# Optimization experiments

Measured on AMD Instinct MI355X. Metric: run time of the kernel, lower is better.

## Reference

```python
import jax, jax.numpy as jnp
import numpy as np

N = 50000   # nodes
E = 640000  # edges (before self-loops)
D = 128     # in_dim == out_dim
H = 4       # heads
C = 32      # per-head channels (out_dim // heads)
ED = 1      # edge_dim
NEG_SLOPE = 0.2
LN_EPS = 1e-5


def setup_inputs() -> dict:
    key = jax.random.key(0)
    ks = jax.random.split(key, 8)
    glorot = lambda k, sh, fan: jax.random.normal(k, sh, jnp.float32) / np.float32(np.sqrt(fan))
    return dict(
        x=jax.random.normal(ks[0], (N, D), jnp.float32),
        edge_index=jax.random.randint(ks[1], (2, E), 0, N, dtype=jnp.int32),
        edge_attr=jax.random.uniform(ks[2], (E, ED), jnp.float32),
        W_l=glorot(ks[3], (D, H * C), D), b_l=jnp.zeros((H * C,), jnp.float32),
        W_r=glorot(ks[4], (D, H * C), D), b_r=jnp.zeros((H * C,), jnp.float32),
        W_e=glorot(ks[5], (ED, H * C), ED),
        att=glorot(ks[6], (H, C), C),
        bias=jnp.zeros((H * C,), jnp.float32),
        ln_gamma=jnp.ones((H * C,), jnp.float32),
        ln_beta=jnp.zeros((H * C,), jnp.float32),
    )


def reference(x, edge_index, edge_attr, W_l, b_l, W_r, b_r, W_e, att, bias, ln_gamma, ln_beta):
    n = x.shape[0]
    src, dst = edge_index[0], edge_index[1]
    # --- add self loops; self-loop edge_attr = mean of incoming attrs (PyG fill_value='mean') ---
    attr_sum = jax.ops.segment_sum(edge_attr, dst, num_segments=n)          # (N, ED)
    cnt = jax.ops.segment_sum(jnp.ones((edge_attr.shape[0], 1), edge_attr.dtype), dst, num_segments=n)
    loop_attr = attr_sum / jnp.maximum(cnt, 1.0)
    ea = jnp.concatenate([edge_attr, loop_attr], axis=0)                    # (E+N, ED)
    loop = jnp.arange(n, dtype=src.dtype)
    src = jnp.concatenate([src, loop])
    dst = jnp.concatenate([dst, loop])
    # --- GATv2: separate source/target linear transforms ---
    x_l = (x @ W_l + b_l).reshape(n, H, C)   # source (x_j)
    x_r = (x @ W_r + b_r).reshape(n, H, C)   # target (x_i)
    e_f = (ea @ W_e).reshape(-1, H, C)       # edge embedding (E+N, H, C)
    xj = x_l[src]                            # gather (E+N, H, C)
    m = jax.nn.leaky_relu(xj + x_r[dst] + e_f, NEG_SLOPE)
    alpha = jnp.einsum('ehc,hc->eh', m, att)
    # --- segment softmax over incoming edges of each target node ---
    amax = jax.ops.segment_max(alpha, dst, num_segments=n)  # every node has a self-loop
    ex = jnp.exp(alpha - amax[dst])
    denom = jax.ops.segment_sum(ex, dst, num_segments=n)
    a = ex / denom[dst]                                     # (E+N, H); attn dropout is eval no-op
    # --- scatter-aggregate messages, concat heads, conv bias ---
    out = jax.ops.segment_sum(xj * a[..., None], dst, num_segments=n).reshape(n, H * C) + bias
    # --- ELU, dropout (eval no-op), residual (in_dim == out_dim, no res_proj), LayerNorm ---
    out = jax.nn.elu(out) + x
    mu = jnp.mean(out, axis=-1, keepdims=True)
    var = jnp.var(out, axis=-1, keepdims=True)
    return (out - mu) * jax.lax.rsqrt(var + LN_EPS) * ln_gamma + ln_beta
```

## Files before the change

kernel.cpp:

```cpp
#include <hip/hip_runtime.h>
#include <hip/hip_fp16.h>
#include <math.h>

#define DCH 128
#define NEG 0.2f
#define LOG2E 1.44269504088896f
#define NPART 256
#define SCAP 20
#define BCAP 1152

typedef _Float16 f16x8 __attribute__((ext_vector_type(8)));
typedef float    f32x4 __attribute__((ext_vector_type(4)));
typedef float    f32x2 __attribute__((ext_vector_type(2)));
typedef unsigned long long u64;

static __device__ __forceinline__ float dpp_radd4(float v) {
    int b;
    b = __builtin_amdgcn_update_dpp(0, __float_as_int(v), 0xB1, 0xF, 0xF, true);
    v += __int_as_float(b);
    b = __builtin_amdgcn_update_dpp(0, __float_as_int(v), 0x4E, 0xF, 0xF, true);
    v += __int_as_float(b);
    return v;
}

__global__ __launch_bounds__(256) void k_prep(
        const float* __restrict__ x, __half* __restrict__ xf16, int total4,
        const float* __restrict__ Wl, const float* __restrict__ Wr,
        __half* __restrict__ wtl, __half* __restrict__ wtr, int nb_cvt) {
    int bid = blockIdx.x;
    if (bid < nb_cvt) {
        int i = bid * 256 + (int)threadIdx.x;
        if (i >= total4) return;
        float4 v = ((const float4*)x)[i];
        __half2* dst = (__half2*)xf16 + 2 * (size_t)i;
        dst[0] = __floats2half2_rn(v.x, v.y);
        dst[1] = __floats2half2_rn(v.z, v.w);
    } else {
        int t = (bid - nb_cvt) * 256 + (int)threadIdx.x;
        if (t >= 2 * DCH * DCH) return;
        const float* W = (t < DCH * DCH) ? Wl : Wr;
        __half* wt = (t < DCH * DCH) ? wtl : wtr;
        int u = t & (DCH * DCH - 1);
        int k = u >> 7, j = u & 127;
        wt[j * 128 + k] = __float2half_rn(W[u]);
    }
}

__global__ __launch_bounds__(256) void k_mmpart(
        const __half* __restrict__ xf16,
        const __half* __restrict__ wtl, const __half* __restrict__ wtr,
        const float* __restrict__ bl, const float* __restrict__ br,
        __half* __restrict__ xl16, float* __restrict__ xro, int N,
        const int* __restrict__ ei, const float* __restrict__ eattr,
        unsigned* __restrict__ sorted, unsigned* __restrict__ cnt,
        int E, int NB, int chunkE, int nb_mm) {
    if ((int)blockIdx.x >= nb_mm) {
        __shared__ unsigned cur[1024];
        int p = (int)blockIdx.x - nb_mm;
        for (int i = threadIdx.x; i < 1024; i += 256) cur[i] = 0u;
        __syncthreads();
        int e0 = p * chunkE;
        int e1 = e0 + chunkE; if (e1 > E) e1 = E;
        for (int e = e0 + (int)threadIdx.x; e < e1; e += 256) {
            int d = ei[E + e], s = ei[e];
            float a = eattr[e];
            int b = d >> 6, dl = d & 63;
            unsigned q = (unsigned)fminf(a * 1024.f + 0.5f, 1023.f);
            unsigned rank = atomicAdd(&cur[b], 1u);
            if (rank < SCAP)
                sorted[((size_t)b * NPART + p) * SCAP + rank] =
                    (unsigned)dl | ((unsigned)s << 6) | (q << 22);
        }
        __syncthreads();
        for (int b = threadIdx.x; b < NB; b += 256) {
            unsigned c = cur[b];
            cnt[(size_t)b * NPART + p] = c < SCAP ? c : SCAP;
        }
        return;
    }
    int wave = threadIdx.x >> 6, lane = threadIdx.x & 63;
    int node0 = blockIdx.x * 64;
    int jbase = wave * 32;
    int rl = lane & 15, kg = lane >> 4;
    f32x4 acc[4][2][2];
    #pragma unroll
    for (int a = 0; a < 4; ++a)
        #pragma unroll
        for (int b = 0; b < 2; ++b)
            #pragma unroll
            for (int c = 0; c < 2; ++c)
                acc[a][b][c] = (f32x4){0.f, 0.f, 0.f, 0.f};
    #pragma unroll
    for (int ks = 0; ks < 4; ++ks) {
        int koff = ks * 32 + kg * 8;
        f16x8 av[4];
        #pragma unroll
        for (int rt = 0; rt < 4; ++rt) {
            int row = node0 + rt * 16 + rl;
            if (row >= N) row = N - 1;
            av[rt] = *(const f16x8*)(xf16 + (size_t)row * 128 + koff);
        }
        #pragma unroll
        for (int jt = 0; jt < 2; ++jt) {
            int j = jbase + jt * 16 + rl;
            size_t ob = (size_t)j * 128 + koff;
            f16x8 bL = *(const f16x8*)(wtl + ob);
            f16x8 bR = *(const f16x8*)(wtr + ob);
            #pragma unroll
            for (int rt = 0; rt < 4; ++rt) {
                acc[rt][jt][0] = __builtin_amdgcn_mfma_f32_16x16x32_f16(av[rt], bL, acc[rt][jt][0], 0, 0, 0);
                acc[rt][jt][1] = __builtin_amdgcn_mfma_f32_16x16x32_f16(av[rt], bR, acc[rt][jt][1], 0, 0, 0);
            }
        }
    }
    float blv[2], brv[2];
    #pragma unroll
    for (int jt = 0; jt < 2; ++jt) {
        int j = jbase + jt * 16 + rl;
        blv[jt] = bl[j]; brv[jt] = br[j];
    }
    #pragma unroll
    for (int rt = 0; rt < 4; ++rt) {
        #pragma unroll
        for (int r = 0; r < 4; ++r) {
            int row = node0 + rt * 16 + kg * 4 + r;
            if (row < N) {
                #pragma unroll
                for (int jt = 0; jt < 2; ++jt) {
                    int j = jbase + jt * 16 + rl;
                    xl16[(size_t)row * 128 + j] = __float2half_rn(acc[rt][jt][0][r] + blv[jt]);
                    xro[(size_t)row * 128 + j] = acc[rt][jt][1][r] + brv[jt];
                }
            }
        }
    }
}

__global__ __launch_bounds__(256) void k_fill2(
        const unsigned* __restrict__ sorted, const unsigned* __restrict__ cnt,
        unsigned* __restrict__ csr, uint2* __restrict__ ndesc,
        float* __restrict__ lattr, int N) {
    __shared__ unsigned lraw[BCAP];
    __shared__ unsigned hcnt[64], qsum[64];
    __shared__ unsigned wsum[4], wpre[5];
    __shared__ int ncur[64];
    __shared__ int tot_s;
    int t = threadIdx.x, lane = t & 63, w = t >> 6;
    int bucket = blockIdx.x;
    if (t < 64) { hcnt[t] = 0u; qsum[t] = 0u; }
    unsigned v = cnt[(size_t)bucket * NPART + t];
    int sc = (int)v;
    #pragma unroll
    for (int o = 1; o < 64; o <<= 1) {
        int tmp = __shfl_up(sc, o, 64);
        if (lane >= o) sc += tmp;
    }
    if (lane == 63) wsum[w] = (unsigned)sc;
    __syncthreads();
    if (t == 0) {
        wpre[0] = 0;
        #pragma unroll
        for (int k = 0; k < 4; ++k) wpre[k + 1] = wpre[k] + wsum[k];
        tot_s = (int)(wpre[4] < BCAP ? wpre[4] : BCAP);
    }
    __syncthreads();
    unsigned sb = wpre[w] + (unsigned)sc - v;
    {
        const unsigned* src = sorted + ((size_t)bucket * NPART + t) * SCAP;
        for (int i = 0; i < (int)v; ++i) {
            unsigned idx = sb + (unsigned)i;
            if (idx < BCAP) {
                unsigned rec = src[i];
                lraw[idx] = rec;
                int dl = (int)(rec & 63u);
                atomicAdd(&hcnt[dl], 1u);
                atomicAdd(&qsum[dl], rec >> 22);
            }
        }
    }
    __syncthreads();
    if (t < 64) {
        int nv = (int)hcnt[t], nsc = nv;
        #pragma unroll
        for (int o = 1; o < 64; o <<= 1) {
            int tmp = __shfl_up(nsc, o, 64);
            if (t >= o) nsc += tmp;
        }
        int nb = nsc - nv;
        ncur[t] = nb;
        int node = bucket * 64 + t;
        if (node < N) {
            ndesc[node] = make_uint2((unsigned)(bucket * BCAP + nb), (unsigned)nv);
            lattr[node] = ((float)qsum[t] * (1.f / 1024.f)) / fmaxf((float)nv, 1.f);
        }
    }
    __syncthreads();
    int tot = tot_s;
    for (int i = t; i < tot; i += 256) {
        unsigned rec = lraw[i];
        int dl = (int)(rec & 63u);
        int pos = atomicAdd(&ncur[dl], 1);
        csr[(size_t)bucket * BCAP + pos] = ((rec >> 6) & 0xFFFFu) | ((rec >> 22) << 16);
    }
}

__global__ __launch_bounds__(256) void k_gat(
        const __half* __restrict__ xl16, const float* __restrict__ xrp, const float* __restrict__ x,
        const unsigned* __restrict__ csr, const uint2* __restrict__ ndesc,
        const float* __restrict__ lattr,
        const float* __restrict__ We, const float* __restrict__ att, const float* __restrict__ bias,
        const float* __restrict__ gamma, const float* __restrict__ beta,
        float* __restrict__ out, int N) {
    int wid = threadIdx.x >> 6;
    int lane = threadIdx.x & 63;
    int node = blockIdx.x * 4 + wid;
    if (node >= N) return;
    int q = lane >> 4;
    int sl = lane & 15;
    int c8 = sl << 3;

    float4 attA = *(const float4*)(att + c8);
    float4 attB = *(const float4*)(att + c8 + 4);
    attA.x *= LOG2E; attA.y *= LOG2E; attA.z *= LOG2E; attA.w *= LOG2E;
    attB.x *= LOG2E; attB.y *= LOG2E; attB.z *= LOG2E; attB.w *= LOG2E;
    float4 weA = *(const float4*)(We + c8);
    float4 weB = *(const float4*)(We + c8 + 4);
    float4 xrA = *(const float4*)(xrp + (size_t)node * 128 + c8);
    float4 xrB = *(const float4*)(xrp + (size_t)node * 128 + c8 + 4);

    uint2 nd = ndesc[node];
    int beg = (int)nd.x, deg = (int)nd.y;
    float la = lattr[node];
    int T = deg + 1;

    float4 accA = {0.f, 0.f, 0.f, 0.f}, accB = {0.f, 0.f, 0.f, 0.f};
    float den = 0.f;

    for (int p = 0; p < T; p += 4) {
        int idx = p + q;
        bool isReal = idx < deg;
        unsigned rec = 0u;
        if (isReal) rec = csr[beg + idx];
        int src = isReal ? (int)(rec & 0xFFFFu) : node;
        float ea = isReal ? (float)(rec >> 16) * (1.f / 1024.f) : la;
        float vmask = (idx <= deg) ? 1.f : 0.f;
        uint4 graw = *(const uint4*)(xl16 + ((size_t)src << 7) + c8);
        float2 g0 = __half22float2(*(const __half2*)&graw.x);
        float2 g1 = __half22float2(*(const __half2*)&graw.y);
        float2 g2 = __half22float2(*(const __half2*)&graw.z);
        float2 g3 = __half22float2(*(const __half2*)&graw.w);
        float t0 = g0.x + fmaf(ea, weA.x, xrA.x); t0 = fmaxf(t0, t0 * NEG);
        float t1 = g0.y + fmaf(ea, weA.y, xrA.y); t1 = fmaxf(t1, t1 * NEG);
        float t2 = g1.x + fmaf(ea, weA.z, xrA.z); t2 = fmaxf(t2, t2 * NEG);
        float t3 = g1.y + fmaf(ea, weA.w, xrA.w); t3 = fmaxf(t3, t3 * NEG);
        float t4 = g2.x + fmaf(ea, weB.x, xrB.x); t4 = fmaxf(t4, t4 * NEG);
        float t5 = g2.y + fmaf(ea, weB.y, xrB.y); t5 = fmaxf(t5, t5 * NEG);
        float t6 = g3.x + fmaf(ea, weB.z, xrB.z); t6 = fmaxf(t6, t6 * NEG);
        float t7 = g3.y + fmaf(ea, weB.w, xrB.w); t7 = fmaxf(t7, t7 * NEG);
        float d = t0 * attA.x;
        d = fmaf(t1, attA.y, d); d = fmaf(t2, attA.z, d); d = fmaf(t3, attA.w, d);
        d = fmaf(t4, attB.x, d); d = fmaf(t5, attB.y, d); d = fmaf(t6, attB.z, d);
        d = fmaf(t7, attB.w, d);
        float pt = dpp_radd4(d);
        float pe = exp2f(pt) * vmask;
        den += pe;
        accA.x = fmaf(pe, g0.x, accA.x); accA.y = fmaf(pe, g0.y, accA.y);
        accA.z = fmaf(pe, g1.x, accA.z); accA.w = fmaf(pe, g1.y, accA.w);
        accB.x = fmaf(pe, g2.x, accB.x); accB.y = fmaf(pe, g2.y, accB.y);
        accB.z = fmaf(pe, g3.x, accB.z); accB.w = fmaf(pe, g3.y, accB.w);
    }

    den += __shfl_xor(den, 16, 64);
    accA.x += __shfl_xor(accA.x, 16, 64); accA.y += __shfl_xor(accA.y, 16, 64);
    accA.z += __shfl_xor(accA.z, 16, 64); accA.w += __shfl_xor(accA.w, 16, 64);
    accB.x += __shfl_xor(accB.x, 16, 64); accB.y += __shfl_xor(accB.y, 16, 64);
    accB.z += __shfl_xor(accB.z, 16, 64); accB.w += __shfl_xor(accB.w, 16, 64);
    den += __shfl_xor(den, 32, 64);
    accA.x += __shfl_xor(accA.x, 32, 64); accA.y += __shfl_xor(accA.y, 32, 64);
    accA.z += __shfl_xor(accA.z, 32, 64); accA.w += __shfl_xor(accA.w, 32, 64);
    accB.x += __shfl_xor(accB.x, 32, 64); accB.y += __shfl_xor(accB.y, 32, 64);
    accB.z += __shfl_xor(accB.z, 32, 64); accB.w += __shfl_xor(accB.w, 32, 64);

    float inv = 1.f / den;
    float4 biA = *(const float4*)(bias + c8);
    float4 biB = *(const float4*)(bias + c8 + 4);
    float o0 = fmaf(accA.x, inv, biA.x), o1 = fmaf(accA.y, inv, biA.y);
    float o2 = fmaf(accA.z, inv, biA.z), o3 = fmaf(accA.w, inv, biA.w);
    float o4 = fmaf(accB.x, inv, biB.x), o5 = fmaf(accB.y, inv, biB.y);
    float o6 = fmaf(accB.z, inv, biB.z), o7 = fmaf(accB.w, inv, biB.w);
    o0 = o0 > 0.f ? o0 : (__expf(o0) - 1.f);
    o1 = o1 > 0.f ? o1 : (__expf(o1) - 1.f);
    o2 = o2 > 0.f ? o2 : (__expf(o2) - 1.f);
    o3 = o3 > 0.f ? o3 : (__expf(o3) - 1.f);
    o4 = o4 > 0.f ? o4 : (__expf(o4) - 1.f);
    o5 = o5 > 0.f ? o5 : (__expf(o5) - 1.f);
    o6 = o6 > 0.f ? o6 : (__expf(o6) - 1.f);
    o7 = o7 > 0.f ? o7 : (__expf(o7) - 1.f);
    float4 xvA = *(const float4*)(x + (size_t)node * 128 + c8);
    float4 xvB = *(const float4*)(x + (size_t)node * 128 + c8 + 4);
    o0 += xvA.x; o1 += xvA.y; o2 += xvA.z; o3 += xvA.w;
    o4 += xvB.x; o5 += xvB.y; o6 += xvB.z; o7 += xvB.w;
    float r1 = ((o0 + o1) + (o2 + o3)) + ((o4 + o5) + (o6 + o7));
    float r2 = o0 * o0;
    r2 = fmaf(o1, o1, r2); r2 = fmaf(o2, o2, r2); r2 = fmaf(o3, o3, r2);
    r2 = fmaf(o4, o4, r2); r2 = fmaf(o5, o5, r2); r2 = fmaf(o6, o6, r2);
    r2 = fmaf(o7, o7, r2);
    #pragma unroll
    for (int mk = 1; mk < 16; mk <<= 1) {
        r1 += __shfl_xor(r1, mk, 16);
        r2 += __shfl_xor(r2, mk, 16);
    }
    float mean = r1 * (1.f / 128.f);
    float var  = r2 * (1.f / 128.f) - mean * mean;
    float rr = rsqrtf(var + 1e-5f);
    if (q == 0) {
        float4 gmA = *(const float4*)(gamma + c8);
        float4 gmB = *(const float4*)(gamma + c8 + 4);
        float4 btA = *(const float4*)(beta + c8);
        float4 btB = *(const float4*)(beta + c8 + 4);
        float4 wA, wB;
        wA.x = (o0 - mean) * rr * gmA.x + btA.x;
        wA.y = (o1 - mean) * rr * gmA.y + btA.y;
        wA.z = (o2 - mean) * rr * gmA.z + btA.z;
        wA.w = (o3 - mean) * rr * gmA.w + btA.w;
        wB.x = (o4 - mean) * rr * gmB.x + btB.x;
        wB.y = (o5 - mean) * rr * gmB.y + btB.y;
        wB.z = (o6 - mean) * rr * gmB.z + btB.z;
        wB.w = (o7 - mean) * rr * gmB.w + btB.w;
        *(float4*)(out + (size_t)node * 128 + c8) = wA;
        *(float4*)(out + (size_t)node * 128 + c8 + 4) = wB;
    }
}

extern "C" void kernel_launch(void* const* d_in, const int* in_sizes, int n_in,
                              void* d_out, int out_size, void* d_ws, size_t ws_size,
                              hipStream_t stream) {
    const float* x     = (const float*)d_in[0];
    const int*   ei    = (const int*)d_in[1];
    const float* eattr = (const float*)d_in[2];
    const float* Wl    = (const float*)d_in[3];
    const float* bl    = (const float*)d_in[4];
    const float* Wr    = (const float*)d_in[5];
    const float* br    = (const float*)d_in[6];
    const float* We    = (const float*)d_in[7];
    const float* att   = (const float*)d_in[8];
    const float* bias  = (const float*)d_in[9];
    const float* gam   = (const float*)d_in[10];
    const float* bet   = (const float*)d_in[11];
    float* out = (float*)d_out;
    int N = in_sizes[0] / DCH;
    int E = in_sizes[1] / 2;
    int NB = (N + 63) / 64;

    char* base = (char*)d_ws;
    size_t off = 0;
    auto alloc = [&](size_t nbytes) -> void* {
        void* p = base + off;
        off += (nbytes + 255) & ~(size_t)255;
        return p;
    };
    unsigned* sorted = (unsigned*)alloc((size_t)NB * NPART * SCAP * 4);
    unsigned* cnt    = (unsigned*)alloc((size_t)NB * NPART * 4);
    unsigned* csr    = (unsigned*)alloc((size_t)NB * BCAP * 4);
    uint2*    ndesc  = (uint2*)alloc((size_t)N * 8);
    float*    lattr  = (float*)alloc((size_t)N * 4);
    __half*   xl16   = (__half*)alloc((size_t)N * DCH * 2);
    float*    xrb    = (float*)alloc((size_t)N * DCH * 4);
    __half*   xf16   = (__half*)alloc((size_t)N * DCH * 2);
    __half*   wtl    = (__half*)alloc((size_t)DCH * DCH * 2);
    __half*   wtr    = (__half*)alloc((size_t)DCH * DCH * 2);
    (void)n_in; (void)out_size; (void)ws_size;

    int total4  = N * DCH / 4;
    int nb_cvt  = (total4 + 255) / 256;
    int nb_cvtw = (2 * DCH * DCH + 255) / 256;
    int nb_mm   = (N + 63) / 64;
    int chunkE  = (E + NPART - 1) / NPART;

    k_prep<<<nb_cvt + nb_cvtw, 256, 0, stream>>>(
        x, xf16, total4, Wl, Wr, wtl, wtr, nb_cvt);
    k_mmpart<<<nb_mm + NPART, 256, 0, stream>>>(
        xf16, wtl, wtr, bl, br, xl16, xrb, N,
        ei, eattr, sorted, cnt, E, NB, chunkE, nb_mm);
    k_fill2<<<NB, 256, 0, stream>>>(
        sorted, cnt, csr, ndesc, lattr, N);
    k_gat<<<(N + 3) / 4, 256, 0, stream>>>(
        xl16, xrb, x, csr, ndesc, lattr, We, att, bias, gam, bet, out, N);
}
```

Measured before the change: 98.76 us.

## Compact partition records via local counting sort and prefetch gathers in GAT loop

The partition blocks now run a two-pass local counting sort in shared memory: they count records per bucket, prefix-sum the counts, write records contiguously into an LDS buffer, and copy that buffer to global memory in one coalesced pass. A per-(bucket,partition) base-offset array replaces the fixed SCAP-slot layout, so the padded, scattered writes go away and per-slot overflow truncation is no longer possible. The GAT edge loop is also software-pipelined, with edge metadata prefetched four iterations ahead and feature gathers three ahead, to hide gather latency. This costs about 22KB more LDS per partition block and extra registers in k_gat, which may lower occupancy.

```diff
diff --git a/kernel.cpp b/kernel.cpp
--- a/kernel.cpp
+++ b/kernel.cpp
@@ -6,13 +6,11 @@
 #define NEG 0.2f
 #define LOG2E 1.44269504088896f
 #define NPART 256
-#define SCAP 20
+#define RCAP 2512
 #define BCAP 1152
 
 typedef _Float16 f16x8 __attribute__((ext_vector_type(8)));
 typedef float    f32x4 __attribute__((ext_vector_type(4)));
-typedef float    f32x2 __attribute__((ext_vector_type(2)));
-typedef unsigned long long u64;
 
 static __device__ __forceinline__ float dpp_radd4(float v) {
     int b;
@@ -53,29 +51,68 @@
         __half* __restrict__ xl16, float* __restrict__ xro, int N,
         const int* __restrict__ ei, const float* __restrict__ eattr,
         unsigned* __restrict__ sorted, unsigned* __restrict__ cnt,
+        unsigned* __restrict__ gbase,
         int E, int NB, int chunkE, int nb_mm) {
     if ((int)blockIdx.x >= nb_mm) {
-        __shared__ unsigned cur[1024];
+        __shared__ unsigned lcnt[1024];
+        __shared__ unsigned lbase[1024];
+        __shared__ unsigned lcur[1024];
+        __shared__ unsigned recbuf[RCAP];
+        __shared__ unsigned wsum2[4], wpre2[5];
         int p = (int)blockIdx.x - nb_mm;
-        for (int i = threadIdx.x; i < 1024; i += 256) cur[i] = 0u;
+        int t = threadIdx.x, lane = t & 63, w = t >> 6;
+        for (int i = t; i < 1024; i += 256) lcnt[i] = 0u;
         __syncthreads();
         int e0 = p * chunkE;
         int e1 = e0 + chunkE; if (e1 > E) e1 = E;
-        for (int e = e0 + (int)threadIdx.x; e < e1; e += 256) {
+        for (int e = e0 + t; e < e1; e += 256)
+            atomicAdd(&lcnt[ei[E + e] >> 6], 1u);
+        __syncthreads();
+        unsigned c0 = lcnt[t * 4 + 0], c1 = lcnt[t * 4 + 1];
+        unsigned c2 = lcnt[t * 4 + 2], c3 = lcnt[t * 4 + 3];
+        unsigned s4 = c0 + c1 + c2 + c3;
+        unsigned sc = s4;
+        #pragma unroll
+        for (int o = 1; o < 64; o <<= 1) {
+            unsigned tmp = __shfl_up(sc, o, 64);
+            if (lane >= o) sc += tmp;
+        }
+        if (lane == 63) wsum2[w] = sc;
+        __syncthreads();
+        if (t == 0) {
+            wpre2[0] = 0;
+            #pragma unroll
+            for (int k = 0; k < 4; ++k) wpre2[k + 1] = wpre2[k] + wsum2[k];
+        }
+        __syncthreads();
+        unsigned base4 = wpre2[w] + sc - s4;
+        lbase[t * 4 + 0] = base4;
+        lbase[t * 4 + 1] = base4 + c0;
+        lbase[t * 4 + 2] = base4 + c0 + c1;
+        lbase[t * 4 + 3] = base4 + c0 + c1 + c2;
+        lcur[t * 4 + 0] = lbase[t * 4 + 0];
+        lcur[t * 4 + 1] = lbase[t * 4 + 1];
+        lcur[t * 4 + 2] = lbase[t * 4 + 2];
+        lcur[t * 4 + 3] = lbase[t * 4 + 3];
+        __syncthreads();
+        unsigned gB = (unsigned)(p * chunkE);
+        for (int b = t; b < NB; b += 256) {
+            cnt[(size_t)b * NPART + p] = lcnt[b];
+            gbase[(size_t)b * NPART + p] = gB + lbase[b];
+        }
+        for (int e = e0 + t; e < e1; e += 256) {
             int d = ei[E + e], s = ei[e];
             float a = eattr[e];
             int b = d >> 6, dl = d & 63;
-            unsigned q = (unsigned)fminf(a * 1024.f + 0.5f, 1023.f);
-            unsigned rank = atomicAdd(&cur[b], 1u);
-            if (rank < SCAP)
-                sorted[((size_t)b * NPART + p) * SCAP + rank] =
-                    (unsigned)dl | ((unsigned)s << 6) | (q << 22);
-        }
-        __syncthreads();
-        for (int b = threadIdx.x; b < NB; b += 256) {
-            unsigned c = cur[b];
-            cnt[(size_t)b * NPART + p] = c < SCAP ? c : SCAP;
-        }
+            unsigned qq = (unsigned)fminf(a * 1024.f + 0.5f, 1023.f);
+            unsigned rank = atomicAdd(&lcur[b], 1u);
+            if (rank < RCAP)
+                recbuf[rank] = (unsigned)dl | ((unsigned)s << 6) | (qq << 22);
+        }
+        __syncthreads();
+        int tot = e1 - e0;
+        for (int i = t; i < tot; i += 256)
+            sorted[(size_t)p * chunkE + i] = recbuf[i];
         return;
     }
     int wave = threadIdx.x >> 6, lane = threadIdx.x & 63;
@@ -138,6 +175,7 @@
 
 __global__ __launch_bounds__(256) void k_fill2(
         const unsigned* __restrict__ sorted, const unsigned* __restrict__ cnt,
+        const unsigned* __restrict__ gbase,
         unsigned* __restrict__ csr, uint2* __restrict__ ndesc,
         float* __restrict__ lattr, int N) {
     __shared__ unsigned lraw[BCAP];
@@ -149,6 +187,7 @@
     int bucket = blockIdx.x;
     if (t < 64) { hcnt[t] = 0u; qsum[t] = 0u; }
     unsigned v = cnt[(size_t)bucket * NPART + t];
+    unsigned gb = gbase[(size_t)bucket * NPART + t];
     int sc = (int)v;
     #pragma unroll
     for (int o = 1; o < 64; o <<= 1) {
@@ -166,7 +205,7 @@
     __syncthreads();
     unsigned sb = wpre[w] + (unsigned)sc - v;
     {
-        const unsigned* src = sorted + ((size_t)bucket * NPART + t) * SCAP;
+        const unsigned* src = sorted + gb;
         for (int i = 0; i < (int)v; ++i) {
             unsigned idx = sb + (unsigned)i;
             if (idx < BCAP) {
@@ -236,38 +275,56 @@
     float4 accA = {0.f, 0.f, 0.f, 0.f}, accB = {0.f, 0.f, 0.f, 0.f};
     float den = 0.f;
 
+    auto meta = [&](int pp, int& ss, float& ea, float& vm) {
+        int idx = pp + q;
+        bool real = idx < deg;
+        unsigned rec = real ? csr[beg + idx] : 0u;
+        ss = real ? (int)(rec & 0xFFFFu) : node;
+        ea = real ? (float)(rec >> 16) * (1.f / 1024.f) : la;
+        vm = (idx <= deg) ? 1.f : 0.f;
+    };
+    auto gth = [&](int ss) -> uint4 {
+        return *(const uint4*)(xl16 + ((size_t)ss << 7) + c8);
+    };
+
+    int sA, sB, sC, sD;
+    float eaA, eaB, eaC, eaD, vA, vB, vC, vD;
+    uint4 gA4, gB4, gC4;
+    meta(0, sA, eaA, vA);
+    meta(4, sB, eaB, vB);
+    meta(8, sC, eaC, vC);
+    meta(12, sD, eaD, vD);
+    gA4 = gth(sA); gB4 = gth(sB); gC4 = gth(sC);
+
     for (int p = 0; p < T; p += 4) {
-        int idx = p + q;
-        bool isReal = idx < deg;
-        unsigned rec = 0u;
-        if (isReal) rec = csr[beg + idx];
-        int src = isReal ? (int)(rec & 0xFFFFu) : node;
-        float ea = isReal ? (float)(rec >> 16) * (1.f / 1024.f) : la;
-        float vmask = (idx <= deg) ? 1.f : 0.f;
-        uint4 graw = *(const uint4*)(xl16 + ((size_t)src << 7) + c8);
-        float2 g0 = __half22float2(*(const __half2*)&graw.x);
-        float2 g1 = __half22float2(*(const __half2*)&graw.y);
-        float2 g2 = __half22float2(*(const __half2*)&graw.z);
-        float2 g3 = __half22float2(*(const __half2*)&graw.w);
-        float t0 = g0.x + fmaf(ea, weA.x, xrA.x); t0 = fmaxf(t0, t0 * NEG);
-        float t1 = g0.y + fmaf(ea, weA.y, xrA.y); t1 = fmaxf(t1, t1 * NEG);
-        float t2 = g1.x + fmaf(ea, weA.z, xrA.z); t2 = fmaxf(t2, t2 * NEG);
-        float t3 = g1.y + fmaf(ea, weA.w, xrA.w); t3 = fmaxf(t3, t3 * NEG);
-        float t4 = g2.x + fmaf(ea, weB.x, xrB.x); t4 = fmaxf(t4, t4 * NEG);
-        float t5 = g2.y + fmaf(ea, weB.y, xrB.y); t5 = fmaxf(t5, t5 * NEG);
-        float t6 = g3.x + fmaf(ea, weB.z, xrB.z); t6 = fmaxf(t6, t6 * NEG);
-        float t7 = g3.y + fmaf(ea, weB.w, xrB.w); t7 = fmaxf(t7, t7 * NEG);
+        float2 g0 = __half22float2(*(const __half2*)&gA4.x);
+        float2 g1 = __half22float2(*(const __half2*)&gA4.y);
+        float2 g2 = __half22float2(*(const __half2*)&gA4.z);
+        float2 g3 = __half22float2(*(const __half2*)&gA4.w);
+        float t0 = g0.x + fmaf(eaA, weA.x, xrA.x); t0 = fmaxf(t0, t0 * NEG);
+        float t1 = g0.y + fmaf(eaA, weA.y, xrA.y); t1 = fmaxf(t1, t1 * NEG);
+        float t2 = g1.x + fmaf(eaA, weA.z, xrA.z); t2 = fmaxf(t2, t2 * NEG);
+        float t3 = g1.y + fmaf(eaA, weA.w, xrA.w); t3 = fmaxf(t3, t3 * NEG);
+        float t4 = g2.x + fmaf(eaA, weB.x, xrB.x); t4 = fmaxf(t4, t4 * NEG);
+        float t5 = g2.y + fmaf(eaA, weB.y, xrB.y); t5 = fmaxf(t5, t5 * NEG);
+        float t6 = g3.x + fmaf(eaA, weB.z, xrB.z); t6 = fmaxf(t6, t6 * NEG);
+        float t7 = g3.y + fmaf(eaA, weB.w, xrB.w); t7 = fmaxf(t7, t7 * NEG);
         float d = t0 * attA.x;
         d = fmaf(t1, attA.y, d); d = fmaf(t2, attA.z, d); d = fmaf(t3, attA.w, d);
         d = fmaf(t4, attB.x, d); d = fmaf(t5, attB.y, d); d = fmaf(t6, attB.z, d);
         d = fmaf(t7, attB.w, d);
         float pt = dpp_radd4(d);
-        float pe = exp2f(pt) * vmask;
+        float pe = exp2f(pt) * vA;
         den += pe;
         accA.x = fmaf(pe, g0.x, accA.x); accA.y = fmaf(pe, g0.y, accA.y);
         accA.z = fmaf(pe, g1.x, accA.z); accA.w = fmaf(pe, g1.y, accA.w);
         accB.x = fmaf(pe, g2.x, accB.x); accB.y = fmaf(pe, g2.y, accB.y);
         accB.z = fmaf(pe, g3.x, accB.z); accB.w = fmaf(pe, g3.y, accB.w);
+        eaA = eaB; vA = vB; gA4 = gB4;
+        eaB = eaC; vB = vC; gB4 = gC4;
+        sC = sD; eaC = eaD; vC = vD;
+        gC4 = gth(sC);
+        meta(p + 16, sD, eaD, vD);
     }
 
     den += __shfl_xor(den, 16, 64);
@@ -359,8 +416,10 @@
         off += (nbytes + 255) & ~(size_t)255;
         return p;
     };
-    unsigned* sorted = (unsigned*)alloc((size_t)NB * NPART * SCAP * 4);
+    int chunkE = (E + NPART - 1) / NPART;
+    unsigned* sorted = (unsigned*)alloc((size_t)NPART * chunkE * 4);
     unsigned* cnt    = (unsigned*)alloc((size_t)NB * NPART * 4);
+    unsigned* gbase  = (unsigned*)alloc((size_t)NB * NPART * 4);
     unsigned* csr    = (unsigned*)alloc((size_t)NB * BCAP * 4);
     uint2*    ndesc  = (uint2*)alloc((size_t)N * 8);
     float*    lattr  = (float*)alloc((size_t)N * 4);
@@ -375,15 +434,14 @@
     int nb_cvt  = (total4 + 255) / 256;
     int nb_cvtw = (2 * DCH * DCH + 255) / 256;
     int nb_mm   = (N + 63) / 64;
-    int chunkE  = (E + NPART - 1) / NPART;
 
     k_prep<<<nb_cvt + nb_cvtw, 256, 0, stream>>>(
         x, xf16, total4, Wl, Wr, wtl, wtr, nb_cvt);
     k_mmpart<<<nb_mm + NPART, 256, 0, stream>>>(
         xf16, wtl, wtr, bl, br, xl16, xrb, N,
-        ei, eattr, sorted, cnt, E, NB, chunkE, nb_mm);
+        ei, eattr, sorted, cnt, gbase, E, NB, chunkE, nb_mm);
     k_fill2<<<NB, 256, 0, stream>>>(
-        sorted, cnt, csr, ndesc, lattr, N);
+        sorted, cnt, gbase, csr, ndesc, lattr, N);
     k_gat<<<(N + 3) / 4, 256, 0, stream>>>(
         xl16, xrb, x, csr, ndesc, lattr, We, att, bias, gam, bet, out, N);
 }
```

After: 105.9 us. 1.07x slower.
